# Performance work log

Measured on AMD Instinct MI355X. Metric: run time of the kernel, lower is better.

Reference implementation:

```python
import jax, jax.numpy as jnp
import numpy as np

B, C_IN, MID, H, W = 4, 512, 512, 50, 50
A = 9
FEAT_STRIDE = 16
IMG = H * FEAT_STRIDE  # 800
N_PRE, N_POST = 1200, 300
NMS_TH = 0.7
MIN_SIZE = 16.0


def _anchor_base(base=16.0, ratios=(0.5, 1.0, 2.0), scales=(8, 16, 32)):
    ab = np.zeros((len(ratios) * len(scales), 4), np.float32)
    py = px = base / 2.0
    for i, r in enumerate(ratios):
        for j, s in enumerate(scales):
            h = base * s * np.sqrt(r)
            w = base * s * np.sqrt(1.0 / r)
            ab[i * len(scales) + j] = [py - h / 2, px - w / 2, py + h / 2, px + w / 2]
    return ab


def _all_anchors():
    ab = _anchor_base()
    sy = np.arange(0, H * FEAT_STRIDE, FEAT_STRIDE, dtype=np.float32)
    sx = np.arange(0, W * FEAT_STRIDE, FEAT_STRIDE, dtype=np.float32)
    SX, SY = np.meshgrid(sx, sy)
    shift = np.stack([SY.ravel(), SX.ravel(), SY.ravel(), SX.ravel()], axis=1)
    return jnp.asarray((shift[:, None, :] + ab[None]).reshape(-1, 4))  # [H*W*A,4]


ANCHORS = _all_anchors()


def _conv(x, w, b, pad):
    y = jax.lax.conv_general_dilated(x, w, (1, 1), [(pad, pad), (pad, pad)],
                                     dimension_numbers=('NCHW', 'OIHW', 'NCHW'))
    return y + b[None, :, None, None]


def _loc2bbox(anc, loc):
    h = anc[:, 2] - anc[:, 0]
    w = anc[:, 3] - anc[:, 1]
    cy = anc[:, 0] + 0.5 * h
    cx = anc[:, 1] + 0.5 * w
    dy, dx, dh, dw = loc[:, 0], loc[:, 1], loc[:, 2], loc[:, 3]
    ncy = dy * h + cy
    ncx = dx * w + cx
    nh = jnp.exp(dh) * h
    nw = jnp.exp(dw) * w
    return jnp.stack([ncy - 0.5 * nh, ncx - 0.5 * nw, ncy + 0.5 * nh, ncx + 0.5 * nw], axis=1)


def _nms_keep(boxes, thresh):
    y1, x1, y2, x2 = boxes[:, 0], boxes[:, 1], boxes[:, 2], boxes[:, 3]
    iy = jnp.clip(jnp.minimum(y2[:, None], y2[None]) - jnp.maximum(y1[:, None], y1[None]), 0.0)
    ix = jnp.clip(jnp.minimum(x2[:, None], x2[None]) - jnp.maximum(x1[:, None], x1[None]), 0.0)
    inter = iy * ix
    area = (y2 - y1) * (x2 - x1)
    iou = inter / (area[:, None] + area[None] - inter + 1e-9)  # [N_PRE,N_PRE]

    def step(carry, i):
        sup, keep = carry
        k = ~sup[i]
        keep = keep.at[i].set(k)
        newsup = jnp.where(k & (iou[i] > thresh), True, sup)
        newsup = newsup.at[i].set(sup[i])
        return (newsup, keep), None

    n = boxes.shape[0]
    init = (jnp.zeros(n, bool), jnp.zeros(n, bool))
    (_, keep), _ = jax.lax.scan(step, init, jnp.arange(n))
    return keep


def _propose(loc, fg):
    roi = _loc2bbox(ANCHORS, loc)
    roi = jnp.stack([jnp.clip(roi[:, 0], 0.0, IMG), jnp.clip(roi[:, 1], 0.0, IMG),
                     jnp.clip(roi[:, 2], 0.0, IMG), jnp.clip(roi[:, 3], 0.0, IMG)], axis=1)
    hs = roi[:, 2] - roi[:, 0]
    ws = roi[:, 3] - roi[:, 1]
    s = jnp.where((hs >= MIN_SIZE) & (ws >= MIN_SIZE), fg, -jnp.inf)
    top_s, top_i = jax.lax.top_k(s, N_PRE)          # score-sorted pre-NMS candidates
    boxes = roi[top_i]
    keep = _nms_keep(boxes, NMS_TH)
    _, sel = jax.lax.top_k(jnp.where(keep, top_s, -jnp.inf), N_POST)
    return boxes[sel]                                # [N_POST,4]


def setup_inputs() -> dict:
    key = jax.random.key(0)
    ks = jax.random.split(key, 4)
    x = jax.random.normal(ks[0], (B, C_IN, H, W), jnp.float32)
    W1 = jax.random.normal(ks[1], (MID, C_IN, 3, 3), jnp.float32) * 0.01
    b1 = jnp.zeros((MID,), jnp.float32)
    Wl = jax.random.normal(ks[2], (A * 4, MID, 1, 1), jnp.float32) * 0.01
    bl = jnp.zeros((A * 4,), jnp.float32)
    Ws = jax.random.normal(ks[3], (A * 2, MID, 1, 1), jnp.float32) * 0.01
    bs = jnp.zeros((A * 2,), jnp.float32)
    return {'x': x, 'W1': W1, 'b1': b1, 'Wl': Wl, 'bl': bl, 'Ws': Ws, 'bs': bs}


def reference(x, W1, b1, Wl, bl, Ws, bs):
    h = jax.nn.relu(_conv(x, W1, b1, 1))
    locs = _conv(h, Wl, bl, 0)     # [B, A*4, H, W]
    scores = _conv(h, Ws, bs, 0)   # [B, A*2, H, W]
    rpn_locs = locs.transpose(0, 2, 3, 1).reshape(B, -1, 4)          # [B, H*W*A, 4]
    sc = scores.transpose(0, 2, 3, 1).reshape(B, H, W, A, 2)
    fg = jax.nn.softmax(sc, axis=-1)[..., 1].reshape(B, -1)          # [B, H*W*A]
    rpn_scores = sc.reshape(B, -1, 2)
    rois = jax.vmap(_propose)(rpn_locs, fg)                          # [B, N_POST, 4]
    return rpn_locs, rpn_scores, rois
```

## Files before the change

### kernel.cpp

```cpp
#include <hip/hip_runtime.h>
#include <math.h>

#define BATCH 4
#define CIN 512
#define MID 512
#define HH 50
#define WW 50
#define HWPIX 2500
#define NPIX 10000
#define NANCH 22500
#define NPRE 1200
#define NPOST 300
#define LOCS_OFF 0
#define SCORES_OFF 360000
#define ROIS_OFF 540000

#define PADW 52
#define PPIX 2704

typedef _Float16 half8 __attribute__((ext_vector_type(8)));
typedef float floatx4 __attribute__((ext_vector_type(4)));

__device__ __forceinline__ void gload16(const void* g, void* l) {
    __builtin_amdgcn_global_load_lds(
        (const __attribute__((address_space(1))) unsigned int*)g,
        (__attribute__((address_space(3))) unsigned int*)l, 16, 0, 0);
}

__device__ __forceinline__ unsigned long long rdlane64(unsigned int lo,
                                                       unsigned int hi, int l) {
    const unsigned int a = (unsigned int)__builtin_amdgcn_readlane((int)lo, l);
    const unsigned int b = (unsigned int)__builtin_amdgcn_readlane((int)hi, l);
    return ((unsigned long long)b << 32) | a;
}


__global__ __launch_bounds__(256) void prep_combo_kernel(
    const float* __restrict__ x, const float* __restrict__ W1,
    const float* __restrict__ Wl, const float* __restrict__ Wsc,
    _Float16* __restrict__ xh, _Float16* __restrict__ xl,
    _Float16* __restrict__ wth, _Float16* __restrict__ wtl,
    float* __restrict__ wh) {
    __shared__ __align__(16) char smem[18432];
    const int blk = blockIdx.x;
    const int t   = threadIdx.x;

    if (blk < 1280) {
        float (*tile)[65] = (float(*)[65])smem;
        const int pt = blk % 40;
        const int ct = (blk / 40) % 8;
        const int b  = blk / 320;
        const int p0 = pt * 64, c0 = ct * 64;

        #pragma unroll
        for (int r = 0; r < 16; ++r) {
            const int cc = (t >> 6) + r * 4;
            const int pp = t & 63;
            const int p  = p0 + pp;
            tile[cc][pp] = (p < HWPIX) ? x[((size_t)b * 512 + c0 + cc) * HWPIX + p] : 0.f;
        }
        __syncthreads();
        #pragma unroll
        for (int r = 0; r < 16; ++r) {
            const int pp = (t >> 6) + r * 4;
            const int cc = t & 63;
            const int p  = p0 + pp;
            if (p < HWPIX) {
                const int y = p / WW, xx2 = p % WW;
                const float v = tile[cc][pp];
                const _Float16 hh = (_Float16)v;
                const float rr = v - (float)hh;
                const _Float16 ll = (_Float16)(rr * 2048.0f);
                const size_t o = ((size_t)(b * PPIX + (y + 1) * PADW + xx2 + 1)) * 512 + c0 + cc;
                xh[o] = hh;
                xl[o] = ll;
            }
        }
    } else {
        const int wblk = blk - 1280;
        if (wblk < 512) {
            float* buf = (float*)smem;
            const int m = wblk;
            const float* src = W1 + (size_t)m * 4608;
            for (int i = t; i < 4608; i += 256) buf[i] = src[i];
            __syncthreads();
            for (int kk = 0; kk < 9; ++kk) {
                for (int c = t; c < 512; c += 256) {
                    const float v = buf[c * 9 + kk];
                    const _Float16 hh = (_Float16)v;
                    const float rr = v - (float)hh;
                    const size_t o = (size_t)kk * 262144 + (size_t)m * 512 + c;
                    wth[o] = hh;
                    wtl[o] = (_Float16)(rr * 2048.0f);
                }
            }
        } else if (wblk < 640) {
            const int g2 = (wblk - 512) * 256 + t;
            const int c = g2 >> 6, n = g2 & 63;
            float v = 0.f;
            if (n < 36)      v = Wl[n * 512 + c];
            else if (n < 54) v = Wsc[(n - 36) * 512 + c];
            wh[g2] = v;
        } else {
            const int idx = (wblk - 640) * 256 + t;
            if (idx < BATCH * PPIX * 4) {
                const int pix = idx >> 2, q = idx & 3;
                const int r = pix % PPIX;
                const int yy = r / PADW, xx2 = r % PADW;
                if (yy == 0 || yy == PADW - 1 || xx2 == 0 || xx2 == PADW - 1) {
                    float4 z = make_float4(0.f, 0.f, 0.f, 0.f);
                    float4* ph = (float4*)(xh + (size_t)pix * 512 + q * 128);
                    float4* pl = (float4*)(xl + (size_t)pix * 512 + q * 128);
                    #pragma unroll
                    for (int i = 0; i < 16; ++i) { ph[i] = z; pl[i] = z; }
                }
            }
        }
    }
}

#define BUFSZ 20480
#define AOFF_L 8192
#define BOFF_H 16384
#define BOFF_L 18432
#define MTILES 80

__global__ __launch_bounds__(256) void conv_mfma_kernel(
    const _Float16* __restrict__ xh, const _Float16* __restrict__ xl,
    const _Float16* __restrict__ wth, const _Float16* __restrict__ wtl,
    const float* __restrict__ b1, float* __restrict__ h) {
    __shared__ __align__(16) char lds[2 * BUFSZ];

    const int bid  = blockIdx.x;
    const int t    = threadIdx.x;
    const int w    = t >> 6;
    const int lane = t & 63;
    const int n0   = (bid / MTILES) * 32;
    const int m0   = (bid % MTILES) * 128;
    const int wq   = w * 1024;

    const int sr = t >> 2;
    const int cp = t & 3;
    const int clA = (cp - (sr >> 1)) & 3;

    int P0 = m0 + sr;       if (P0 > NPIX - 1) P0 = NPIX - 1;
    int P1 = m0 + sr + 64;  if (P1 > NPIX - 1) P1 = NPIX - 1;
    const int b0 = P0 / HWPIX, pl0 = P0 % HWPIX;
    const int b1i = P1 / HWPIX, pl1 = P1 % HWPIX;
    const int baseA0 = ((b0 * PPIX) + (pl0 / WW + 1) * PADW + (pl0 % WW + 1)) * 512 + clA * 8;
    const int baseA1 = ((b1i * PPIX) + (pl1 / WW + 1) * PADW + (pl1 % WW + 1)) * 512 + clA * 8;

    const int wb  = (w < 2) ? w : (w - 2);
    const int rB  = wb * 16 + (lane >> 2);
    const int cpB = lane & 3;
    const int clB = (cpB - (rB >> 1)) & 3;
    const int baseB = (n0 + rB) * 512 + clB * 8;

    const int lr = lane & 15, lq = lane >> 4;
    const int wrow = w * 32;
    const int rA0 = wrow + lr, rA1 = wrow + 16 + lr;
    const int offA0 = rA0 * 64 + (((lq + (rA0 >> 1)) & 3) << 4);
    const int offA1 = rA1 * 64 + (((lq + (rA1 >> 1)) & 3) << 4);
    int offB[2];
    #pragma unroll
    for (int ctl = 0; ctl < 2; ++ctl) {
        const int rBf = ctl * 16 + lr;
        offB[ctl] = rBf * 64 + (((lq + (rBf >> 1)) & 3) << 4);
    }

    floatx4 acc1[2][2] = {};
    floatx4 acc2[2][2] = {};

    auto issue = [&](int u) {
        char* D = lds + ((u & 1) ? BUFSZ : 0);
        const int kk = u >> 4, ct = u & 15;
        const int kd = kk / 3;
        const int dA = ((kd - 1) * PADW + (kk - kd * 3 - 1)) * 512 + ct * 32;
        const int dB = kk * 262144 + ct * 32;
        gload16(xh + baseA0 + dA, D + 0 + wq);
        gload16(xh + baseA1 + dA, D + 4096 + wq);
        gload16(xl + baseA0 + dA, D + AOFF_L + wq);
        gload16(xl + baseA1 + dA, D + AOFF_L + 4096 + wq);
        if (w < 2) gload16(wth + baseB + dB, D + BOFF_H + wb * 1024);
        else       gload16(wtl + baseB + dB, D + BOFF_L + wb * 1024);
    };

    issue(0);
    for (int s = 0; s < 144; ++s) {
        __syncthreads();
        if (s + 1 < 144) issue(s + 1);
        const char* Bb = lds + ((s & 1) ? BUFSZ : 0);
        const half8 afh0 = *(const half8*)(Bb + offA0);
        const half8 afh1 = *(const half8*)(Bb + offA1);
        const half8 afl0 = *(const half8*)(Bb + AOFF_L + offA0);
        const half8 afl1 = *(const half8*)(Bb + AOFF_L + offA1);
        #pragma unroll
        for (int ctl = 0; ctl < 2; ++ctl) {
            const half8 bfh = *(const half8*)(Bb + BOFF_H + offB[ctl]);
            const half8 bfl = *(const half8*)(Bb + BOFF_L + offB[ctl]);
            acc1[0][ctl] = __builtin_amdgcn_mfma_f32_16x16x32_f16(afh0, bfh, acc1[0][ctl], 0, 0, 0);
            acc2[0][ctl] = __builtin_amdgcn_mfma_f32_16x16x32_f16(afh0, bfl, acc2[0][ctl], 0, 0, 0);
            acc2[0][ctl] = __builtin_amdgcn_mfma_f32_16x16x32_f16(afl0, bfh, acc2[0][ctl], 0, 0, 0);
            acc1[1][ctl] = __builtin_amdgcn_mfma_f32_16x16x32_f16(afh1, bfh, acc1[1][ctl], 0, 0, 0);
            acc2[1][ctl] = __builtin_amdgcn_mfma_f32_16x16x32_f16(afh1, bfl, acc2[1][ctl], 0, 0, 0);
            acc2[1][ctl] = __builtin_amdgcn_mfma_f32_16x16x32_f16(afl1, bfh, acc2[1][ctl], 0, 0, 0);
        }
    }

    const float s2 = 1.0f / 2048.0f;
    #pragma unroll
    for (int rt = 0; rt < 2; ++rt) {
        #pragma unroll
        for (int ctl = 0; ctl < 2; ++ctl) {
            const int m = n0 + ctl * 16 + lr;
            const float bias = b1[m];
            #pragma unroll
            for (int r = 0; r < 4; ++r) {
                const int P = m0 + wrow + rt * 16 + lq * 4 + r;
                if (P < NPIX) {
                    const float v = acc1[rt][ctl][r] + acc2[rt][ctl][r] * s2 + bias;
                    h[(size_t)P * 512 + m] = fmaxf(v, 0.f);
                }
            }
        }
    }
}

__global__ void wt_kernel(const float* __restrict__ W1,
                          const float* __restrict__ Wl,
                          const float* __restrict__ Wsc,
                          float* __restrict__ w1t, float* __restrict__ wh) {
    int g = blockIdx.x * 256 + threadIdx.x;
    if (g < 9 * 512 * 512) {
        int kk = g / (512 * 512);
        int r  = g % (512 * 512);
        int c  = r / 512;
        int m  = r % 512;
        w1t[g] = W1[(size_t)m * 4608 + c * 9 + kk];
    } else {
        int g2 = g - 9 * 512 * 512;
        if (g2 < 512 * 64) {
            int c = g2 >> 6, n = g2 & 63;
            float v = 0.f;
            if (n < 36)      v = Wl[n * 512 + c];
            else if (n < 54) v = Wsc[(n - 36) * 512 + c];
            wh[g2] = v;
        }
    }
}

__global__ __launch_bounds__(256) void conv3x3_fallback(
    const float* __restrict__ x, const float* __restrict__ w1t,
    const float* __restrict__ b1, float* __restrict__ h) {
    __shared__ float As[16][64];
    __shared__ float Bs[16][64];
    const int t  = threadIdx.x;
    const int tx = t & 15;
    const int ty = t >> 4;
    const int m0 = blockIdx.x * 64;
    const int n0 = blockIdx.y * 64;
    const int pix = t & 63;
    const int cl0 = t >> 6;
    const int P  = m0 + pix;
    const bool vp = (P < NPIX);
    const int b  = P / HWPIX;
    const int pl = P % HWPIX;
    const int yy = pl / WW;
    const int xx = pl % WW;
    float acc[4][4] = {};
    for (int kk = 0; kk < 9; ++kk) {
        const int ky = kk / 3 - 1, kx = kk % 3 - 1;
        const int y2 = yy + ky, x2 = xx + kx;
        const bool v = vp && ((unsigned)y2 < (unsigned)HH) && ((unsigned)x2 < (unsigned)WW);
        const float* xbase = x + (size_t)b * CIN * HWPIX + y2 * WW + x2;
        const float* wbase = w1t + (size_t)kk * 512 * 512 + n0;
        for (int ct = 0; ct < 512 / 16; ++ct) {
            __syncthreads();
            #pragma unroll
            for (int r = 0; r < 4; ++r) {
                const int cl = cl0 + r * 4;
                const int c  = ct * 16 + cl;
                As[cl][pix] = v ? xbase[(size_t)c * HWPIX] : 0.f;
                Bs[cl][pix] = wbase[c * 512 + pix];
            }
            __syncthreads();
            #pragma unroll
            for (int k = 0; k < 16; ++k) {
                const float4 a4 = *reinterpret_cast<const float4*>(&As[k][ty * 4]);
                const float4 b4 = *reinterpret_cast<const float4*>(&Bs[k][tx * 4]);
                const float av[4] = {a4.x, a4.y, a4.z, a4.w};
                const float bv[4] = {b4.x, b4.y, b4.z, b4.w};
                #pragma unroll
                for (int i = 0; i < 4; ++i)
                    #pragma unroll
                    for (int j = 0; j < 4; ++j)
                        acc[i][j] = fmaf(av[i], bv[j], acc[i][j]);
            }
        }
    }
    #pragma unroll
    for (int i = 0; i < 4; ++i) {
        const int Pp = m0 + ty * 4 + i;
        if (Pp >= NPIX) continue;
        const int m = n0 + tx * 4;
        float4 o;
        o.x = fmaxf(acc[i][0] + b1[m + 0], 0.f);
        o.y = fmaxf(acc[i][1] + b1[m + 1], 0.f);
        o.z = fmaxf(acc[i][2] + b1[m + 2], 0.f);
        o.w = fmaxf(acc[i][3] + b1[m + 3], 0.f);
        *reinterpret_cast<float4*>(&h[(size_t)Pp * 512 + m]) = o;
    }
}


__global__ __launch_bounds__(256) void heads_kernel(
    const float* __restrict__ h, const float* __restrict__ wh,
    const float* __restrict__ bl, const float* __restrict__ bsc,
    float* __restrict__ out, float* __restrict__ fgb) {
    __shared__ float As[16][17];
    __shared__ float Bs[16][64];
    const int t  = threadIdx.x;
    const int p  = t & 15;
    const int g  = t >> 4;
    const int p0 = blockIdx.x * 16;

    float acc[4] = {0.f, 0.f, 0.f, 0.f};

    for (int ct = 0; ct < 32; ++ct) {
        const int c0 = ct * 16;
        __syncthreads();
        {
            const int pp = t >> 4, cc = t & 15;
            const int PP = p0 + pp;
            As[cc][pp] = (PP < NPIX) ? h[(size_t)PP * 512 + c0 + cc] : 0.f;
            #pragma unroll
            for (int r = 0; r < 4; ++r) {
                const int row = (t >> 6) + 4 * r;
                Bs[row][t & 63] = wh[(size_t)(c0 + row) * 64 + (t & 63)];
            }
        }
        __syncthreads();
        #pragma unroll
        for (int k = 0; k < 16; ++k) {
            const float a = As[k][p];
            const float4 b4 = *reinterpret_cast<const float4*>(&Bs[k][g * 4]);
            acc[0] = fmaf(a, b4.x, acc[0]);
            acc[1] = fmaf(a, b4.y, acc[1]);
            acc[2] = fmaf(a, b4.z, acc[2]);
            acc[3] = fmaf(a, b4.w, acc[3]);
        }
    }

    const int P = p0 + p;
    if (P >= NPIX) return;
    const int b  = P / HWPIX;
    const int pl = P % HWPIX;
    const int n  = g * 4;
    const size_t abase = (size_t)b * NANCH + (size_t)pl * 9;
    if (n < 36) {
        const int a = g;
        float4 o;
        o.x = acc[0] + bl[n + 0];
        o.y = acc[1] + bl[n + 1];
        o.z = acc[2] + bl[n + 2];
        o.w = acc[3] + bl[n + 3];
        *reinterpret_cast<float4*>(&out[LOCS_OFF + (abase + a) * 4]) = o;
    } else if (n < 54) {
        const int ns = n - 36;
        float* so = out + SCORES_OFF;
        {
            const float s0 = acc[0] + bsc[ns + 0];
            const float s1 = acc[1] + bsc[ns + 1];
            const int a0 = ns >> 1;
            so[(abase + a0) * 2 + 0] = s0;
            so[(abase + a0) * 2 + 1] = s1;
            const float mx = fmaxf(s0, s1);
            const float e0 = expf(s0 - mx);
            const float e1 = expf(s1 - mx);
            fgb[abase + a0] = e1 / (e0 + e1);
        }
        if (ns + 3 < 18) {
            const float s0 = acc[2] + bsc[ns + 2];
            const float s1 = acc[3] + bsc[ns + 3];
            const int a1 = (ns >> 1) + 1;
            so[(abase + a1) * 2 + 0] = s0;
            so[(abase + a1) * 2 + 1] = s1;
            const float mx = fmaxf(s0, s1);
            const float e0 = expf(s0 - mx);
            const float e1 = expf(s1 - mx);
            fgb[abase + a1] = e1 / (e0 + e1);
        }
    }
}

__global__ void proposal_prep(const float* __restrict__ out,
                              const float* __restrict__ fgb,
                              float* __restrict__ roi_all,
                              unsigned long long* __restrict__ keys) {
    #pragma clang fp contract(off)
    const int j = blockIdx.x * 256 + threadIdx.x;
    const int b = blockIdx.y;
    if (j >= NANCH) return;

    const int a = j % 9;
    const int p = j / 9;
    const int y = p / WW;
    const int x = p % WW;
    const int ri = a / 3, si = a % 3;
    const double rr[3] = {0.5, 1.0, 2.0};
    const double ss[3] = {8.0, 16.0, 32.0};
    const double hh = 16.0 * ss[si] * sqrt(rr[ri]);
    const double wd = 16.0 * ss[si] * sqrt(1.0 / rr[ri]);
    const float ab0 = (float)(8.0 - hh / 2.0);
    const float ab1 = (float)(8.0 - wd / 2.0);
    const float ab2 = (float)(8.0 + hh / 2.0);
    const float ab3 = (float)(8.0 + wd / 2.0);
    const float sy = (float)(y * 16);
    const float sx = (float)(x * 16);
    const float ay1 = sy + ab0;
    const float ax1 = sx + ab1;
    const float ay2 = sy + ab2;
    const float ax2 = sx + ab3;

    const float h  = ay2 - ay1;
    const float w  = ax2 - ax1;
    const float cy = ay1 + 0.5f * h;
    const float cx = ax1 + 0.5f * w;

    const float* L = out + LOCS_OFF + ((size_t)b * NANCH + j) * 4;
    const float dy = L[0], dx = L[1], dh = L[2], dw = L[3];

    const float ncy = dy * h + cy;
    const float ncx = dx * w + cx;
    const float nh  = expf(dh) * h;
    const float nw  = expf(dw) * w;

    float r0 = ncy - 0.5f * nh;
    float r1 = ncx - 0.5f * nw;
    float r2 = ncy + 0.5f * nh;
    float r3 = ncx + 0.5f * nw;
    r0 = fminf(fmaxf(r0, 0.f), 800.f);
    r1 = fminf(fmaxf(r1, 0.f), 800.f);
    r2 = fminf(fmaxf(r2, 0.f), 800.f);
    r3 = fminf(fmaxf(r3, 0.f), 800.f);

    const float hs  = r2 - r0;
    const float wsz = r3 - r1;
    const float fg  = fgb[(size_t)b * NANCH + j];
    const float s   = (hs >= 16.f && wsz >= 16.f) ? fg : -__builtin_huge_valf();

    float4 ro;
    ro.x = r0; ro.y = r1; ro.z = r2; ro.w = r3;
    *reinterpret_cast<float4*>(&roi_all[((size_t)b * NANCH + j) * 4]) = ro;

    unsigned int bits = __float_as_uint(s);
    unsigned int o = (bits & 0x80000000u) ? ~bits : (bits | 0x80000000u);
    keys[(size_t)b * NANCH + j] =
        ((unsigned long long)o << 32) | (unsigned int)(~(unsigned int)j);
}

__global__ __launch_bounds__(1024) void select_sort_kernel(
    const unsigned long long* __restrict__ keys,
    const float* __restrict__ roi_all, float* __restrict__ boxes) {
    const int b   = blockIdx.x;
    const int tid = threadIdx.x;
    const unsigned long long* K = keys + (size_t)b * NANCH;

    __shared__ unsigned int hist[256][4];
    __shared__ unsigned int suf[256];
    __shared__ unsigned long long sbuf[2048];
    __shared__ unsigned int prefix_s;
    __shared__ int rank_s;
    __shared__ int cnt_s;

    const int sub = (tid >> 8) & 3;

    if (tid == 0) { prefix_s = 0u; rank_s = NPRE; }
    __syncthreads();

    for (int pass = 0; pass < 4; ++pass) {
        for (int i = tid; i < 1024; i += 1024) ((unsigned int*)hist)[i] = 0;
        __syncthreads();
        const unsigned pref = prefix_s;
        for (int i = tid; i < NANCH; i += 1024) {
            const unsigned hk = (unsigned)(K[i] >> 32);
            const bool match = (pass == 0) || ((hk >> (32 - 8 * pass)) == pref);
            if (match) atomicAdd(&hist[(hk >> (24 - 8 * pass)) & 255u][sub], 1u);
        }
        __syncthreads();
        if (tid < 256)
            suf[tid] = hist[tid][0] + hist[tid][1] + hist[tid][2] + hist[tid][3];
        __syncthreads();
        for (int st = 1; st < 256; st <<= 1) {
            unsigned v = 0;
            if (tid < 256) v = suf[tid] + ((tid + st < 256) ? suf[tid + st] : 0u);
            __syncthreads();
            if (tid < 256) suf[tid] = v;
            __syncthreads();
        }
        const int r = rank_s;
        __syncthreads();
        if (tid < 256) {
            const unsigned s_here = suf[tid];
            const unsigned s_up   = (tid < 255) ? suf[tid + 1] : 0u;
            if (s_here >= (unsigned)r && s_up < (unsigned)r) {
                rank_s = r - (int)s_up;
                prefix_s = (prefix_s << 8) | (unsigned)tid;
            }
        }
        __syncthreads();
    }

    const unsigned kth32 = prefix_s;
    if (tid == 0) cnt_s = 0;
    __syncthreads();
    for (int i = tid; i < NANCH; i += 1024) {
        const unsigned long long k = K[i];
        if ((unsigned)(k >> 32) >= kth32) {
            const int p = atomicAdd(&cnt_s, 1);
            if (p < 2048) sbuf[p] = k;
        }
    }
    __syncthreads();
    const int cnt = cnt_s;
    for (int i = tid; i < 2048; i += 1024)
        if (i >= cnt) sbuf[i] = 0ULL;

    for (int ksz = 2; ksz <= 2048; ksz <<= 1) {
        for (int jj = ksz >> 1; jj > 0; jj >>= 1) {
            __syncthreads();
            for (int i = tid; i < 2048; i += 1024) {
                const int l = i ^ jj;
                if (l > i) {
                    const unsigned long long a = sbuf[i];
                    const unsigned long long c = sbuf[l];
                    const bool asc = (i & ksz) != 0;
                    const bool sw  = asc ? (a > c) : (a < c);
                    if (sw) { sbuf[i] = c; sbuf[l] = a; }
                }
            }
        }
    }
    __syncthreads();

    for (int r = tid; r < NPRE; r += 1024) {
        const unsigned long long k = sbuf[r];
        const unsigned int idx = ~((unsigned int)k);
        const float4 v = *reinterpret_cast<const float4*>(
            &roi_all[((size_t)b * NANCH + idx) * 4]);
        *reinterpret_cast<float4*>(&boxes[((size_t)b * NPRE + r) * 4]) = v;
    }
}

__global__ __launch_bounds__(64) void iou_kernel(
    const float* __restrict__ boxes, unsigned long long* __restrict__ mask) {
    #pragma clang fp contract(off)
    const int rb = blockIdx.x;
    const int b  = blockIdx.y;
    const int t  = threadIdx.x;
    __shared__ float bx[NPRE * 4];
    __shared__ float ar[NPRE];

    for (int i = t; i < NPRE * 4; i += 64)
        bx[i] = boxes[(size_t)b * NPRE * 4 + i];
    __syncthreads();
    for (int i = t; i < NPRE; i += 64)
        ar[i] = (bx[i * 4 + 2] - bx[i * 4 + 0]) * (bx[i * 4 + 3] - bx[i * 4 + 1]);
    __syncthreads();

    const int i = rb * 64 + t;
    if (i >= NPRE) return;
    const float y1 = bx[i * 4 + 0], x1 = bx[i * 4 + 1];
    const float y2 = bx[i * 4 + 2], x2 = bx[i * 4 + 3];
    const float ai = ar[i];
    for (int jw = 0; jw < 19; ++jw) {
        unsigned long long bits = 0ULL;
        const int jmax = (jw * 64 + 64 <= NPRE) ? 64 : (NPRE - jw * 64);
        for (int jb = 0; jb < jmax; ++jb) {
            const int j = jw * 64 + jb;
            const float iy = fmaxf(fminf(y2, bx[j * 4 + 2]) - fmaxf(y1, bx[j * 4 + 0]), 0.f);
            const float ix = fmaxf(fminf(x2, bx[j * 4 + 3]) - fmaxf(x1, bx[j * 4 + 1]), 0.f);
            const float inter = iy * ix;
            const float den = ((ai + ar[j]) - inter) + 1e-9f;
            const float iou = inter / den;
            if (iou > 0.7f) bits |= (1ULL << jb);
        }
        mask[((size_t)b * NPRE + i) * 19 + jw] = bits;
    }
}

__global__ __launch_bounds__(64) void nms_scan_kernel(
    const unsigned long long* __restrict__ mask,
    const float* __restrict__ boxes, float* __restrict__ out_rois) {
    const int b    = blockIdx.x;
    const int lane = threadIdx.x;
    const unsigned long long* M = mask + (size_t)b * NPRE * 19;

    __shared__ unsigned long long tile[2][1216];
    __shared__ unsigned long long kw[19];
    __shared__ int sel[NPOST];

    const int lw = (lane < 19) ? lane : 0;

    {
        unsigned long long pre[19];
        #pragma unroll
        for (int q = 0; q < 19; ++q) pre[q] = M[q * 64 + lane];
        #pragma unroll
        for (int q = 0; q < 19; ++q) tile[0][q * 64 + lane] = pre[q];
    }
    __syncthreads();

    unsigned long long sup = 0ULL;

    for (int w = 0; w < 19; ++w) {
        const int cur = w & 1;
        unsigned long long pre[19];
        if (w + 1 < 19) {
            const int gb = (w + 1) * 1216;
            #pragma unroll
            for (int q = 0; q < 19; ++q) pre[q] = M[gb + q * 64 + lane];
        }

        const int nrows = (w == 18) ? (NPRE - 18 * 64) : 64;
        const unsigned long long* tp = tile[cur];

        const unsigned long long diag = (lane < nrows) ? tp[lane * 19 + w] : 0ULL;
        const unsigned int dlo = (unsigned int)diag;
        const unsigned int dhi = (unsigned int)(diag >> 32);

        const unsigned long long ext =
            rdlane64((unsigned int)sup, (unsigned int)(sup >> 32), w);

        unsigned long long sup_in = ext, keep = 0ULL;
        for (int i = 0; i < nrows; ++i) {
            const unsigned long long di = rdlane64(dlo, dhi, i);
            if (!((sup_in >> i) & 1ULL)) {
                keep |= (1ULL << i);
                sup_in |= di;
            }
        }

        #pragma unroll
        for (int i = 0; i < 64; ++i) {
            const unsigned long long mi = tp[i * 19 + lw];
            sup |= mi & (0ULL - ((keep >> i) & 1ULL));
        }

        if (lane == 0) kw[w] = keep;

        if (w + 1 < 19) {
            #pragma unroll
            for (int q = 0; q < 19; ++q) tile[1 - cur][q * 64 + lane] = pre[q];
        }
        __syncthreads();
    }

    int total = 0;
    #pragma unroll
    for (int w = 0; w < 19; ++w) total += __popcll(kw[w]);

    int pref = 0;
    #pragma unroll
    for (int w = 0; w < 19; ++w) {
        const unsigned long long kwv = kw[w];
        const int i = w * 64 + lane;
        const int kr = pref + __popcll(kwv & ((1ULL << lane) - 1ULL));
        if (i < NPRE) {
            if ((kwv >> lane) & 1ULL) {
                if (kr < NPOST) sel[kr] = i;
            } else {
                const int r2 = total + (i - kr);
                if (r2 < NPOST) sel[r2] = i;
            }
        }
        pref += __popcll(kwv);
    }
    __syncthreads();

    for (int rr = lane; rr < NPOST; rr += 64) {
        const int i = sel[rr];
        const float4 v = *reinterpret_cast<const float4*>(
            &boxes[((size_t)b * NPRE + i) * 4]);
        *reinterpret_cast<float4*>(&out_rois[((size_t)b * NPOST + rr) * 4]) = v;
    }
}

extern "C" void kernel_launch(void* const* d_in, const int* in_sizes, int n_in,
                              void* d_out, int out_size, void* d_ws, size_t ws_size,
                              hipStream_t stream) {
    const float* x   = (const float*)d_in[0];
    const float* W1  = (const float*)d_in[1];
    const float* b1  = (const float*)d_in[2];
    const float* Wl  = (const float*)d_in[3];
    const float* bl  = (const float*)d_in[4];
    const float* Wsc = (const float*)d_in[5];
    const float* bsc = (const float*)d_in[6];
    float* out = (float*)d_out;
    char* ws = (char*)d_ws;

    const size_t MAIN_BYTES = 52199424ULL;

    if (ws_size >= MAIN_BYTES) {
        float*    h    = (float*)(ws);
        _Float16* xh   = (_Float16*)(ws + 20480000);
        _Float16* xl   = (_Float16*)(ws + 31555584);
        _Float16* wth  = (_Float16*)(ws + 42631168);
        _Float16* wtl  = (_Float16*)(ws + 47349760);
        float*    wh   = (float*)(ws + 52068352);
        char* alias = ws + 20480000;
        float* fgb  = (float*)(alias);
        float* roi  = (float*)(alias + 360000);
        unsigned long long* keys = (unsigned long long*)(alias + 1800000);
        float* boxes = (float*)(alias + 2520000);
        unsigned long long* mask = (unsigned long long*)(alias + 2596800);

        hipLaunchKernelGGL(prep_combo_kernel, dim3(1280 + 512 + 128 + 169), dim3(256), 0, stream,
                           x, W1, Wl, Wsc, xh, xl, wth, wtl, wh);
        hipLaunchKernelGGL(conv_mfma_kernel, dim3(16 * MTILES), dim3(256), 0, stream,
                           xh, xl, wth, wtl, b1, h);
        hipLaunchKernelGGL(heads_kernel, dim3(625), dim3(256), 0, stream,
                           h, wh, bl, bsc, out, fgb);
        hipLaunchKernelGGL(proposal_prep, dim3((NANCH + 255) / 256, BATCH), dim3(256), 0, stream,
                           out, fgb, roi, keys);
        hipLaunchKernelGGL(select_sort_kernel, dim3(BATCH), dim3(1024), 0, stream,
                           keys, roi, boxes);
        hipLaunchKernelGGL(iou_kernel, dim3(19, BATCH), dim3(64), 0, stream,
                           boxes, mask);
        hipLaunchKernelGGL(nms_scan_kernel, dim3(BATCH), dim3(64), 0, stream,
                           mask, boxes, out + ROIS_OFF);
    } else {
        float* fws = (float*)ws;
        float* w1t     = fws;
        float* h       = w1t + 2359296;
        float* fgb     = h + 5120000;
        float* wh      = fgb + 90000;
        float* roi     = wh + 32768;
        unsigned long long* keys = (unsigned long long*)(roi + 360000);
        float* boxes   = (float*)(keys + 90000);
        unsigned long long* mask = (unsigned long long*)(boxes + 19200);

        hipLaunchKernelGGL(wt_kernel, dim3((9 * 512 * 512 + 512 * 64 + 255) / 256),
                           dim3(256), 0, stream, W1, Wl, Wsc, w1t, wh);
        hipLaunchKernelGGL(conv3x3_fallback, dim3((NPIX + 63) / 64, 512 / 64), dim3(256), 0, stream,
                           x, w1t, b1, h);
        hipLaunchKernelGGL(heads_kernel, dim3(625), dim3(256), 0, stream,
                           h, wh, bl, bsc, out, fgb);
        hipLaunchKernelGGL(proposal_prep, dim3((NANCH + 255) / 256, BATCH), dim3(256), 0, stream,
                           out, fgb, roi, keys);
        hipLaunchKernelGGL(select_sort_kernel, dim3(BATCH), dim3(1024), 0, stream,
                           keys, roi, boxes);
        hipLaunchKernelGGL(iou_kernel, dim3(19, BATCH), dim3(64), 0, stream,
                           boxes, mask);
        hipLaunchKernelGGL(nms_scan_kernel, dim3(BATCH), dim3(64), 0, stream,
                           mask, boxes, out + ROIS_OFF);
    }
}
```

Before: 618.6 us.

## Widen conv N-tile to 64, add split-K partials, fuse proposal prep into heads

The MFMA conv block now computes a 128x64 output tile instead of 128x32, which doubles B-tile reuse per A load. When the workspace is large enough, the K dimension is split across two blocks that write separate partial buffers, keeping the grid at 1280 blocks. Bias and ReLU move into the heads kernel, which sums the two partials on load. The heads kernel also absorbs proposal_prep, computing boxes and sort keys from foreground scores held in shared memory, so one launch and the fgb round trip go away. In exchange, split-K writes an extra 20 MB partial buffer that heads must read back, and the wider tile uses more accumulator registers.

```diff
diff --git a/kernel.cpp b/kernel.cpp
--- a/kernel.cpp
+++ b/kernel.cpp
@@ -119,29 +119,34 @@
     }
 }
 
-#define BUFSZ 20480
+#define BUFSZ 24576
 #define AOFF_L 8192
 #define BOFF_H 16384
-#define BOFF_L 18432
+#define BOFF_L 20480
 #define MTILES 80
 
 __global__ __launch_bounds__(256) void conv_mfma_kernel(
     const _Float16* __restrict__ xh, const _Float16* __restrict__ xl,
     const _Float16* __restrict__ wth, const _Float16* __restrict__ wtl,
-    const float* __restrict__ b1, float* __restrict__ h) {
+    float* __restrict__ hp, int ksplit) {
     __shared__ __align__(16) char lds[2 * BUFSZ];
 
     const int bid  = blockIdx.x;
     const int t    = threadIdx.x;
     const int w    = t >> 6;
     const int lane = t & 63;
-    const int n0   = (bid / MTILES) * 32;
     const int m0   = (bid % MTILES) * 128;
+    const int rr_  = bid / MTILES;
+    int n0, s0, send, kh;
+    if (ksplit) { n0 = (rr_ >> 1) * 64; kh = rr_ & 1; s0 = kh * 72; send = s0 + 72; }
+    else        { n0 = rr_ * 64;        kh = 0;       s0 = 0;       send = 144; }
+    float* hout = hp + (size_t)kh * 5120000;
     const int wq   = w * 1024;
 
     const int sr = t >> 2;
     const int cp = t & 3;
     const int clA = (cp - (sr >> 1)) & 3;
+    const int clB = clA;
 
     int P0 = m0 + sr;       if (P0 > NPIX - 1) P0 = NPIX - 1;
     int P1 = m0 + sr + 64;  if (P1 > NPIX - 1) P1 = NPIX - 1;
@@ -149,27 +154,22 @@
     const int b1i = P1 / HWPIX, pl1 = P1 % HWPIX;
     const int baseA0 = ((b0 * PPIX) + (pl0 / WW + 1) * PADW + (pl0 % WW + 1)) * 512 + clA * 8;
     const int baseA1 = ((b1i * PPIX) + (pl1 / WW + 1) * PADW + (pl1 % WW + 1)) * 512 + clA * 8;
-
-    const int wb  = (w < 2) ? w : (w - 2);
-    const int rB  = wb * 16 + (lane >> 2);
-    const int cpB = lane & 3;
-    const int clB = (cpB - (rB >> 1)) & 3;
-    const int baseB = (n0 + rB) * 512 + clB * 8;
+    const int baseB  = (n0 + sr) * 512 + clB * 8;
 
     const int lr = lane & 15, lq = lane >> 4;
     const int wrow = w * 32;
     const int rA0 = wrow + lr, rA1 = wrow + 16 + lr;
     const int offA0 = rA0 * 64 + (((lq + (rA0 >> 1)) & 3) << 4);
     const int offA1 = rA1 * 64 + (((lq + (rA1 >> 1)) & 3) << 4);
-    int offB[2];
+    int offB[4];
     #pragma unroll
-    for (int ctl = 0; ctl < 2; ++ctl) {
-        const int rBf = ctl * 16 + lr;
-        offB[ctl] = rBf * 64 + (((lq + (rBf >> 1)) & 3) << 4);
-    }
-
-    floatx4 acc1[2][2] = {};
-    floatx4 acc2[2][2] = {};
+    for (int ctl = 0; ctl < 4; ++ctl) {
+        const int rB = ctl * 16 + lr;
+        offB[ctl] = rB * 64 + (((lq + (rB >> 1)) & 3) << 4);
+    }
+
+    floatx4 acc1[2][4] = {};
+    floatx4 acc2[2][4] = {};
 
     auto issue = [&](int u) {
         char* D = lds + ((u & 1) ? BUFSZ : 0);
@@ -181,21 +181,21 @@
         gload16(xh + baseA1 + dA, D + 4096 + wq);
         gload16(xl + baseA0 + dA, D + AOFF_L + wq);
         gload16(xl + baseA1 + dA, D + AOFF_L + 4096 + wq);
-        if (w < 2) gload16(wth + baseB + dB, D + BOFF_H + wb * 1024);
-        else       gload16(wtl + baseB + dB, D + BOFF_L + wb * 1024);
+        gload16(wth + baseB + dB, D + BOFF_H + wq);
+        gload16(wtl + baseB + dB, D + BOFF_L + wq);
     };
 
-    issue(0);
-    for (int s = 0; s < 144; ++s) {
-        __syncthreads();
-        if (s + 1 < 144) issue(s + 1);
+    issue(s0);
+    for (int s = s0; s < send; ++s) {
+        __syncthreads();
+        if (s + 1 < send) issue(s + 1);
         const char* Bb = lds + ((s & 1) ? BUFSZ : 0);
         const half8 afh0 = *(const half8*)(Bb + offA0);
         const half8 afh1 = *(const half8*)(Bb + offA1);
         const half8 afl0 = *(const half8*)(Bb + AOFF_L + offA0);
         const half8 afl1 = *(const half8*)(Bb + AOFF_L + offA1);
         #pragma unroll
-        for (int ctl = 0; ctl < 2; ++ctl) {
+        for (int ctl = 0; ctl < 4; ++ctl) {
             const half8 bfh = *(const half8*)(Bb + BOFF_H + offB[ctl]);
             const half8 bfl = *(const half8*)(Bb + BOFF_L + offB[ctl]);
             acc1[0][ctl] = __builtin_amdgcn_mfma_f32_16x16x32_f16(afh0, bfh, acc1[0][ctl], 0, 0, 0);
@@ -211,16 +211,13 @@
     #pragma unroll
     for (int rt = 0; rt < 2; ++rt) {
         #pragma unroll
-        for (int ctl = 0; ctl < 2; ++ctl) {
+        for (int ctl = 0; ctl < 4; ++ctl) {
             const int m = n0 + ctl * 16 + lr;
-            const float bias = b1[m];
             #pragma unroll
             for (int r = 0; r < 4; ++r) {
                 const int P = m0 + wrow + rt * 16 + lq * 4 + r;
-                if (P < NPIX) {
-                    const float v = acc1[rt][ctl][r] + acc2[rt][ctl][r] * s2 + bias;
-                    h[(size_t)P * 512 + m] = fmaxf(v, 0.f);
-                }
+                if (P < NPIX)
+                    hout[(size_t)P * 512 + m] = acc1[rt][ctl][r] + acc2[rt][ctl][r] * s2;
             }
         }
     }
@@ -251,7 +248,7 @@
 
 __global__ __launch_bounds__(256) void conv3x3_fallback(
     const float* __restrict__ x, const float* __restrict__ w1t,
-    const float* __restrict__ b1, float* __restrict__ h) {
+    float* __restrict__ h) {
     __shared__ float As[16][64];
     __shared__ float Bs[16][64];
     const int t  = threadIdx.x;
@@ -304,21 +301,25 @@
         if (Pp >= NPIX) continue;
         const int m = n0 + tx * 4;
         float4 o;
-        o.x = fmaxf(acc[i][0] + b1[m + 0], 0.f);
-        o.y = fmaxf(acc[i][1] + b1[m + 1], 0.f);
-        o.z = fmaxf(acc[i][2] + b1[m + 2], 0.f);
-        o.w = fmaxf(acc[i][3] + b1[m + 3], 0.f);
+        o.x = acc[i][0];
+        o.y = acc[i][1];
+        o.z = acc[i][2];
+        o.w = acc[i][3];
         *reinterpret_cast<float4*>(&h[(size_t)Pp * 512 + m]) = o;
     }
 }
 
 
 __global__ __launch_bounds__(256) void heads_kernel(
-    const float* __restrict__ h, const float* __restrict__ wh,
+    const float* __restrict__ h0, const float* __restrict__ h1,
+    const float* __restrict__ wh, const float* __restrict__ b1,
     const float* __restrict__ bl, const float* __restrict__ bsc,
-    float* __restrict__ out, float* __restrict__ fgb) {
+    float* __restrict__ out, float* __restrict__ roi_all,
+    unsigned long long* __restrict__ keys) {
+    #pragma clang fp contract(off)
     __shared__ float As[16][17];
     __shared__ float Bs[16][64];
+    __shared__ float fgs[16][9];
     const int t  = threadIdx.x;
     const int p  = t & 15;
     const int g  = t >> 4;
@@ -332,7 +333,14 @@
         {
             const int pp = t >> 4, cc = t & 15;
             const int PP = p0 + pp;
-            As[cc][pp] = (PP < NPIX) ? h[(size_t)PP * 512 + c0 + cc] : 0.f;
+            float v = 0.f;
+            if (PP < NPIX) {
+                const size_t o = (size_t)PP * 512 + c0 + cc;
+                v = h0[o];
+                if (h1) v += h1[o];
+                v = fmaxf(v + b1[c0 + cc], 0.f);
+            }
+            As[cc][pp] = v;
             #pragma unroll
             for (int r = 0; r < 4; ++r) {
                 const int row = (t >> 6) + 4 * r;
@@ -351,21 +359,21 @@
         }
     }
 
-    const int P = p0 + p;
-    if (P >= NPIX) return;
-    const int b  = P / HWPIX;
-    const int pl = P % HWPIX;
+    const int P  = p0 + p;
+    const int b  = (P < NPIX) ? (P / HWPIX) : 0;
+    const int pl = (P < NPIX) ? (P % HWPIX) : 0;
     const int n  = g * 4;
     const size_t abase = (size_t)b * NANCH + (size_t)pl * 9;
-    if (n < 36) {
-        const int a = g;
-        float4 o;
-        o.x = acc[0] + bl[n + 0];
-        o.y = acc[1] + bl[n + 1];
-        o.z = acc[2] + bl[n + 2];
-        o.w = acc[3] + bl[n + 3];
-        *reinterpret_cast<float4*>(&out[LOCS_OFF + (abase + a) * 4]) = o;
-    } else if (n < 54) {
+    const bool vP = (P < NPIX);
+
+    float4 locv = make_float4(0.f, 0.f, 0.f, 0.f);
+    if (vP && n < 36) {
+        locv.x = acc[0] + bl[n + 0];
+        locv.y = acc[1] + bl[n + 1];
+        locv.z = acc[2] + bl[n + 2];
+        locv.w = acc[3] + bl[n + 3];
+        *reinterpret_cast<float4*>(&out[LOCS_OFF + (abase + g) * 4]) = locv;
+    } else if (vP && n < 54) {
         const int ns = n - 36;
         float* so = out + SCORES_OFF;
         {
@@ -377,7 +385,7 @@
             const float mx = fmaxf(s0, s1);
             const float e0 = expf(s0 - mx);
             const float e1 = expf(s1 - mx);
-            fgb[abase + a0] = e1 / (e0 + e1);
+            fgs[p][a0] = e1 / (e0 + e1);
         }
         if (ns + 3 < 18) {
             const float s0 = acc[2] + bsc[ns + 2];
@@ -388,75 +396,66 @@
             const float mx = fmaxf(s0, s1);
             const float e0 = expf(s0 - mx);
             const float e1 = expf(s1 - mx);
-            fgb[abase + a1] = e1 / (e0 + e1);
-        }
-    }
-}
-
-__global__ void proposal_prep(const float* __restrict__ out,
-                              const float* __restrict__ fgb,
-                              float* __restrict__ roi_all,
-                              unsigned long long* __restrict__ keys) {
-    #pragma clang fp contract(off)
-    const int j = blockIdx.x * 256 + threadIdx.x;
-    const int b = blockIdx.y;
-    if (j >= NANCH) return;
-
-    const int a = j % 9;
-    const int p = j / 9;
-    const int y = p / WW;
-    const int x = p % WW;
-    const int ri = a / 3, si = a % 3;
-    const double rr[3] = {0.5, 1.0, 2.0};
-    const double ss[3] = {8.0, 16.0, 32.0};
-    const double hh = 16.0 * ss[si] * sqrt(rr[ri]);
-    const double wd = 16.0 * ss[si] * sqrt(1.0 / rr[ri]);
-    const float ab0 = (float)(8.0 - hh / 2.0);
-    const float ab1 = (float)(8.0 - wd / 2.0);
-    const float ab2 = (float)(8.0 + hh / 2.0);
-    const float ab3 = (float)(8.0 + wd / 2.0);
-    const float sy = (float)(y * 16);
-    const float sx = (float)(x * 16);
-    const float ay1 = sy + ab0;
-    const float ax1 = sx + ab1;
-    const float ay2 = sy + ab2;
-    const float ax2 = sx + ab3;
-
-    const float h  = ay2 - ay1;
-    const float w  = ax2 - ax1;
-    const float cy = ay1 + 0.5f * h;
-    const float cx = ax1 + 0.5f * w;
-
-    const float* L = out + LOCS_OFF + ((size_t)b * NANCH + j) * 4;
-    const float dy = L[0], dx = L[1], dh = L[2], dw = L[3];
-
-    const float ncy = dy * h + cy;
-    const float ncx = dx * w + cx;
-    const float nh  = expf(dh) * h;
-    const float nw  = expf(dw) * w;
-
-    float r0 = ncy - 0.5f * nh;
-    float r1 = ncx - 0.5f * nw;
-    float r2 = ncy + 0.5f * nh;
-    float r3 = ncx + 0.5f * nw;
-    r0 = fminf(fmaxf(r0, 0.f), 800.f);
-    r1 = fminf(fmaxf(r1, 0.f), 800.f);
-    r2 = fminf(fmaxf(r2, 0.f), 800.f);
-    r3 = fminf(fmaxf(r3, 0.f), 800.f);
-
-    const float hs  = r2 - r0;
-    const float wsz = r3 - r1;
-    const float fg  = fgb[(size_t)b * NANCH + j];
-    const float s   = (hs >= 16.f && wsz >= 16.f) ? fg : -__builtin_huge_valf();
-
-    float4 ro;
-    ro.x = r0; ro.y = r1; ro.z = r2; ro.w = r3;
-    *reinterpret_cast<float4*>(&roi_all[((size_t)b * NANCH + j) * 4]) = ro;
-
-    unsigned int bits = __float_as_uint(s);
-    unsigned int o = (bits & 0x80000000u) ? ~bits : (bits | 0x80000000u);
-    keys[(size_t)b * NANCH + j] =
-        ((unsigned long long)o << 32) | (unsigned int)(~(unsigned int)j);
+            fgs[p][a1] = e1 / (e0 + e1);
+        }
+    }
+    __syncthreads();
+
+    if (vP && n < 36) {
+        const int a = g;
+        const int j = pl * 9 + a;
+        const int y = pl / WW;
+        const int x = pl % WW;
+        const int ri = a / 3, si = a % 3;
+        const double rrd[3] = {0.5, 1.0, 2.0};
+        const double ssd[3] = {8.0, 16.0, 32.0};
+        const double hh = 16.0 * ssd[si] * sqrt(rrd[ri]);
+        const double wd = 16.0 * ssd[si] * sqrt(1.0 / rrd[ri]);
+        const float ab0 = (float)(8.0 - hh / 2.0);
+        const float ab1 = (float)(8.0 - wd / 2.0);
+        const float ab2 = (float)(8.0 + hh / 2.0);
+        const float ab3 = (float)(8.0 + wd / 2.0);
+        const float sy = (float)(y * 16);
+        const float sx = (float)(x * 16);
+        const float ay1 = sy + ab0;
+        const float ax1 = sx + ab1;
+        const float ay2 = sy + ab2;
+        const float ax2 = sx + ab3;
+
+        const float h  = ay2 - ay1;
+        const float w  = ax2 - ax1;
+        const float cy = ay1 + 0.5f * h;
+        const float cx = ax1 + 0.5f * w;
+
+        const float dy = locv.x, dx = locv.y, dh = locv.z, dw = locv.w;
+        const float ncy = dy * h + cy;
+        const float ncx = dx * w + cx;
+        const float nh  = expf(dh) * h;
+        const float nw  = expf(dw) * w;
+
+        float r0 = ncy - 0.5f * nh;
+        float r1 = ncx - 0.5f * nw;
+        float r2 = ncy + 0.5f * nh;
+        float r3 = ncx + 0.5f * nw;
+        r0 = fminf(fmaxf(r0, 0.f), 800.f);
+        r1 = fminf(fmaxf(r1, 0.f), 800.f);
+        r2 = fminf(fmaxf(r2, 0.f), 800.f);
+        r3 = fminf(fmaxf(r3, 0.f), 800.f);
+
+        const float hs  = r2 - r0;
+        const float wsz = r3 - r1;
+        const float fg  = fgs[p][a];
+        const float s   = (hs >= 16.f && wsz >= 16.f) ? fg : -__builtin_huge_valf();
+
+        float4 ro;
+        ro.x = r0; ro.y = r1; ro.z = r2; ro.w = r3;
+        *reinterpret_cast<float4*>(&roi_all[((size_t)b * NANCH + j) * 4]) = ro;
+
+        unsigned int bits = __float_as_uint(s);
+        unsigned int o = (bits & 0x80000000u) ? ~bits : (bits | 0x80000000u);
+        keys[(size_t)b * NANCH + j] =
+            ((unsigned long long)o << 32) | (unsigned int)(~(unsigned int)j);
+    }
 }
 
 __global__ __launch_bounds__(1024) void select_sort_kernel(
@@ -699,30 +698,45 @@
     float* out = (float*)d_out;
     char* ws = (char*)d_ws;
 
-    const size_t MAIN_BYTES = 52199424ULL;
-
-    if (ws_size >= MAIN_BYTES) {
-        float*    h    = (float*)(ws);
-        _Float16* xh   = (_Float16*)(ws + 20480000);
-        _Float16* xl   = (_Float16*)(ws + 31555584);
-        _Float16* wth  = (_Float16*)(ws + 42631168);
-        _Float16* wtl  = (_Float16*)(ws + 47349760);
-        float*    wh   = (float*)(ws + 52068352);
-        char* alias = ws + 20480000;
-        float* fgb  = (float*)(alias);
-        float* roi  = (float*)(alias + 360000);
-        unsigned long long* keys = (unsigned long long*)(alias + 1800000);
-        float* boxes = (float*)(alias + 2520000);
-        unsigned long long* mask = (unsigned long long*)(alias + 2596800);
+    const size_t T_A = 72679424ULL;
+    const size_t T_B = 52199424ULL;
+
+    if (ws_size >= T_B) {
+        const bool ksplit = (ws_size >= T_A);
+        float*    h0;
+        float*    h1 = nullptr;
+        _Float16 *xh, *xl, *wth, *wtl;
+        float*    wh;
+        char*     alias;
+        if (ksplit) {
+            h0  = (float*)(ws);
+            h1  = (float*)(ws + 20480000);
+            xh  = (_Float16*)(ws + 40960000);
+            xl  = (_Float16*)(ws + 52035584);
+            wth = (_Float16*)(ws + 63111168);
+            wtl = (_Float16*)(ws + 67829760);
+            wh  = (float*)(ws + 72548352);
+            alias = ws + 40960000;
+        } else {
+            h0  = (float*)(ws);
+            xh  = (_Float16*)(ws + 20480000);
+            xl  = (_Float16*)(ws + 31555584);
+            wth = (_Float16*)(ws + 42631168);
+            wtl = (_Float16*)(ws + 47349760);
+            wh  = (float*)(ws + 52068352);
+            alias = ws + 20480000;
+        }
+        float* roi   = (float*)(alias);
+        unsigned long long* keys = (unsigned long long*)(alias + 1440000);
+        float* boxes = (float*)(alias + 2160000);
+        unsigned long long* mask = (unsigned long long*)(alias + 2236800);
 
         hipLaunchKernelGGL(prep_combo_kernel, dim3(1280 + 512 + 128 + 169), dim3(256), 0, stream,
                            x, W1, Wl, Wsc, xh, xl, wth, wtl, wh);
-        hipLaunchKernelGGL(conv_mfma_kernel, dim3(16 * MTILES), dim3(256), 0, stream,
-                           xh, xl, wth, wtl, b1, h);
+        hipLaunchKernelGGL(conv_mfma_kernel, dim3((ksplit ? 16 : 8) * MTILES), dim3(256), 0, stream,
+                           xh, xl, wth, wtl, h0, (int)(ksplit ? 1 : 0));
         hipLaunchKernelGGL(heads_kernel, dim3(625), dim3(256), 0, stream,
-                           h, wh, bl, bsc, out, fgb);
-        hipLaunchKernelGGL(proposal_prep, dim3((NANCH + 255) / 256, BATCH), dim3(256), 0, stream,
-                           out, fgb, roi, keys);
+                           h0, h1, wh, b1, bl, bsc, out, roi, keys);
         hipLaunchKernelGGL(select_sort_kernel, dim3(BATCH), dim3(1024), 0, stream,
                            keys, roi, boxes);
         hipLaunchKernelGGL(iou_kernel, dim3(19, BATCH), dim3(64), 0, stream,
@@ -730,24 +744,20 @@
         hipLaunchKernelGGL(nms_scan_kernel, dim3(BATCH), dim3(64), 0, stream,
                            mask, boxes, out + ROIS_OFF);
     } else {
-        float* fws = (float*)ws;
-        float* w1t     = fws;
-        float* h       = w1t + 2359296;
-        float* fgb     = h + 5120000;
-        float* wh      = fgb + 90000;
-        float* roi     = wh + 32768;
-        unsigned long long* keys = (unsigned long long*)(roi + 360000);
-        float* boxes   = (float*)(keys + 90000);
-        unsigned long long* mask = (unsigned long long*)(boxes + 19200);
+        float* w1t = (float*)(ws);
+        float* h   = (float*)(ws + 9437184);
+        float* wh  = (float*)(ws + 29917184);
+        float* roi = (float*)(ws + 30048256);
+        unsigned long long* keys = (unsigned long long*)(ws + 31488256);
+        float* boxes = (float*)(ws + 32208256);
+        unsigned long long* mask = (unsigned long long*)(ws + 32285056);
 
         hipLaunchKernelGGL(wt_kernel, dim3((9 * 512 * 512 + 512 * 64 + 255) / 256),
                            dim3(256), 0, stream, W1, Wl, Wsc, w1t, wh);
         hipLaunchKernelGGL(conv3x3_fallback, dim3((NPIX + 63) / 64, 512 / 64), dim3(256), 0, stream,
-                           x, w1t, b1, h);
+                           x, w1t, h);
         hipLaunchKernelGGL(heads_kernel, dim3(625), dim3(256), 0, stream,
-                           h, wh, bl, bsc, out, fgb);
-        hipLaunchKernelGGL(proposal_prep, dim3((NANCH + 255) / 256, BATCH), dim3(256), 0, stream,
-                           out, fgb, roi, keys);
+                           h, (const float*)nullptr, wh, b1, bl, bsc, out, roi, keys);
         hipLaunchKernelGGL(select_sort_kernel, dim3(BATCH), dim3(1024), 0, stream,
                            keys, roi, boxes);
         hipLaunchKernelGGL(iou_kernel, dim3(19, BATCH), dim3(64), 0, stream,
```

Result: faster. 540.6 us (-12.6%).
